# Optimization experiments

Hardware: AMD Instinct MI355X
Metric: run time of the kernel (lower is better)

## Reference

```python
import jax, jax.numpy as jnp
import numpy as np

B, N, D, R, W, H, I = 256, 2048, 128, 4, 1, 1024, 1024
CI = I + R * D                       # controller input size (1536)
IF = 2 * D * W + 2 * W + 1 + 4 * R + D * R   # interface size (787)
OPI = H + R * D                      # output_proj input (1536)


def _norm(v):
    # F.normalize(dim=-1): x / max(||x||, eps)
    return v / jnp.maximum(jnp.linalg.norm(v, axis=-1, keepdims=True), 1e-12)


def setup_inputs() -> dict:
    key = jax.random.key(0)
    ks = jax.random.split(key, 16)
    u = lambda k, shape, fan: jax.random.uniform(k, shape, jnp.float32, -1.0 / np.sqrt(fan), 1.0 / np.sqrt(fan))
    return {
        "x": jax.random.normal(ks[0], (B, I), jnp.float32),
        "memory": jax.random.normal(ks[1], (N, D), jnp.float32) * np.sqrt(2.0 / (N + D)),  # xavier-ish
        "usage": jax.random.uniform(ks[2], (N,), jnp.float32),          # usage in [0,1)
        "link": jax.random.normal(ks[3], (N, N), jnp.float32) * 0.01,   # non-trivial link state
        "W_ih": u(ks[4], (4 * H, CI), H),
        "W_hh": u(ks[5], (4 * H, H), H),
        "b_ih": u(ks[6], (4 * H,), H),
        "b_hh": u(ks[7], (4 * H,), H),
        "W_if": u(ks[8], (IF, H), H),
        "b_if": u(ks[9], (IF,), H),
        "W_out": u(ks[10], (H, OPI), OPI),
        "b_out": u(ks[11], (H,), OPI),
    }


def reference(x, memory, usage, link, W_ih, W_hh, b_ih, b_hh, W_if, b_if, W_out, b_out):
    # initial uniform read weights (prev state at first step)
    prev_rw = jnp.full((B, R, N), 1.0 / N, x.dtype)
    read_flat = (prev_rw @ memory).reshape(B, -1)                 # (B, R*D)
    cin = jnp.concatenate([x, read_flat], axis=-1)                # (B, CI)

    # single LSTM step, h0 = c0 = 0, torch gate order i,f,g,o
    g = cin @ W_ih.T + b_ih + b_hh
    gi, gf, gg, go = jnp.split(g, 4, axis=-1)
    c = jax.nn.sigmoid(gi) * jnp.tanh(gg)
    h = jax.nn.sigmoid(go) * jnp.tanh(c)                          # (B, H) controller out

    itf = h @ W_if.T + b_if                                       # (B, IF)
    o = 0
    write_vals = itf[:, o:o + D * W].reshape(B, W, D); o += D * W
    erase = jax.nn.sigmoid(itf[:, o:o + D * W]).reshape(B, W, D); o += D * W
    write_gates = jax.nn.sigmoid(itf[:, o:o + W]); o += W         # (B, W)
    alloc_gate = jax.nn.sigmoid(itf[:, o:o + 1]); o += 1          # (B, 1)
    o += W                                                        # free gates (parsed, unused)
    read_modes = jax.nn.softmax(itf[:, o:o + 3 * R].reshape(B, R, 3), -1); o += 3 * R
    read_str = jax.nn.softplus(itf[:, o:o + R]); o += R           # (B, R)
    read_keys = itf[:, o:o + D * R].reshape(B, R, D)

    # content addressing for the write (strength = 1)
    mem_n = _norm(memory)
    cw = jax.nn.softmax(_norm(write_vals.mean(1)) @ mem_n.T, -1)  # (B, N)

    # allocation weighting: sorted-usage cumprod (per source semantics)
    idx = jnp.argsort(usage)
    su = usage[idx]
    cp = jnp.cumprod(1.0 - su)
    alloc_s = jnp.concatenate([su[:1], su[1:] * cp[:-1]])
    alloc = jnp.zeros_like(usage).at[idx].set(alloc_s)[None, :] * alloc_gate  # (B, N)

    write_w = write_gates[:, :, None] * (0.5 * cw + 0.5 * alloc)[:, None, :]  # (B, W, N)

    # temporal link update: batch-mean of diag-masked outer product, decay 0.9
    lu = jnp.einsum('bwn,bwm->nm', write_w, write_w) / B
    lu = lu * (1.0 - jnp.eye(N, dtype=lu.dtype))
    link_new = link * 0.9 + lu * 0.1

    # memory write (erase then add, batch-mean)
    ev = erase * write_gates[:, :, None]
    av = write_vals * write_gates[:, :, None]
    erase_mat = jnp.einsum('bwn,bwd->nd', write_w, ev) / B
    add_mat = jnp.einsum('bwn,bwd->nd', write_w, av) / B
    mem_new = memory * (1.0 - erase_mat) + add_mat

    # read addressing on updated memory and updated link (all R heads vectorized)
    sim = jnp.einsum('brd,nd->brn', _norm(read_keys), _norm(mem_new))
    content_r = jax.nn.softmax(sim * read_str[:, :, None], -1)    # (B, R, N)
    backward_w = jnp.einsum('brn,nm->brm', prev_rw, link_new)     # mode 1: prev @ L
    forward_w = jnp.einsum('brn,mn->brm', prev_rw, link_new)      # mode 2: prev @ L^T
    new_rw = (read_modes[..., 0:1] * content_r
              + read_modes[..., 1:2] * backward_w
              + read_modes[..., 2:3] * forward_w)                 # (B, R, N)

    read_out = (new_rw @ mem_new).reshape(B, -1)                  # (B, R*D)
    out = jnp.concatenate([h, read_out], axis=-1) @ W_out.T + b_out
    return out
```

## Files before the change

### kernel.cpp

```cpp
#include <hip/hip_runtime.h>
#include <cmath>

#define DEVI __device__ __forceinline__

DEVI float sigm(float x){ return 1.f/(1.f+expf(-x)); }

typedef __attribute__((ext_vector_type(8))) _Float16 half8;
typedef __attribute__((ext_vector_type(4))) _Float16 half4;
typedef __attribute__((ext_vector_type(4))) float float4v;


__global__ void k_zero(float* __restrict__ p, int n){
  int i = blockIdx.x*256 + threadIdx.x;
  if (i < n) p[i] = 0.f;
}

__global__ __launch_bounds__(256) void k_stage1(
    const float* __restrict__ mem, float* __restrict__ cm, _Float16* __restrict__ mem_h)
{
  __shared__ float smem[4][132];
  const int blk = blockIdx.x, t = threadIdx.x;
  const int wv = t >> 6, lane = t & 63;
  int rbase = blk*16 + wv*4;
  float x0[4], x1[4], ss[4];
  #pragma unroll
  for (int u = 0; u < 4; u++){
    const float* a = mem + (size_t)(rbase+u)*128;
    x0[u] = a[lane]; x1[u] = a[lane+64];
  }
  #pragma unroll
  for (int u = 0; u < 4; u++) ss[u] = x0[u]*x0[u] + x1[u]*x1[u];
  #pragma unroll
  for (int o = 1; o < 64; o <<= 1){
    #pragma unroll
    for (int u = 0; u < 4; u++) ss[u] += __shfl_xor(ss[u], o);
  }
  float c0 = 0.f, c1 = 0.f;
  #pragma unroll
  for (int u = 0; u < 4; u++){
    float invn = 1.f / fmaxf(sqrtf(ss[u]), 1e-12f);
    mem_h[(size_t)(rbase+u)*128 + lane]      = (_Float16)(x0[u]*invn);
    mem_h[(size_t)(rbase+u)*128 + 64 + lane] = (_Float16)(x1[u]*invn);
    c0 += x0[u]; c1 += x1[u];
  }
  smem[wv][lane] = c0; smem[wv][64+lane] = c1;
  __syncthreads();
  if (t < 128) atomicAdd(&cm[t], smem[0][t]+smem[1][t]+smem[2][t]+smem[3][t]);
}

#define QA 264
#define QB 520
#define QB3 776

template<typename TB> struct BReg;
template<> struct BReg<_Float16>{
  half8 v;
  DEVI void load(const _Float16* p){ v = *(const half8*)p; }
  DEVI half8 get() const { return v; }
};
template<> struct BReg<float>{
  float4v a, b;
  DEVI void load(const float* p){ a = *(const float4v*)p; b = *(const float4v*)(p+4); }
  DEVI half8 get() const {
    half8 h;
    #pragma unroll
    for (int j = 0; j < 4; j++){ h[j] = (_Float16)a[j]; h[4+j] = (_Float16)b[j]; }
    return h;
  }
};

struct ARegX {
  float4v a, b; float sc;
  DEVI void load(const float* __restrict__ x, const float* __restrict__ cm, int row, int k){
    const float* p;
    if (k < 1024){ p = x + (size_t)row*1024 + k; sc = 1.f; }
    else         { p = cm + ((k - 1024) & 127); sc = (1.f/2048.f); }
    a = *(const float4v*)p; b = *(const float4v*)(p+4);
  }
  DEVI half8 get() const {
    half8 h;
    #pragma unroll
    for (int j = 0; j < 4; j++){ h[j] = (_Float16)(a[j]*sc); h[4+j] = (_Float16)(b[j]*sc); }
    return h;
  }
};

template<typename TB>
__global__ __launch_bounds__(256) void gemm_t(
    const _Float16* __restrict__ A, const TB* __restrict__ Bm, float* __restrict__ C,
    int M, int N, int K,
    const float* __restrict__ bias1, const float* __restrict__ bias2)
{
  __shared__ _Float16 Ah[2][8*QA];
  __shared__ _Float16 Bh[2][8*QB];
  const int tid = threadIdx.x;
  const int m0 = blockIdx.y*32, n0 = blockIdx.x*64;
  const int T = K >> 6;
  const int arow = tid >> 3, aq = tid & 7;
  const int brow = tid >> 3, bq = tid & 7;
  int nB0 = n0 + brow;      if (nB0 >= N) nB0 = N - 1;
  int nB1 = n0 + brow + 32; if (nB1 >= N) nB1 = N - 1;
  const _Float16* Aptr = A + (size_t)(m0 + arow)*K + aq*8;
  const TB* Bp0 = Bm + (size_t)nB0*K + bq*8;
  const TB* Bp1 = Bm + (size_t)nB1*K + bq*8;
  const int wA  = aq*QA + arow*8;
  const int wB0 = bq*QB + brow*8;
  const int wB1 = bq*QB + (brow+32)*8;
  const int wv_ = tid >> 6, lane = tid & 63;
  const int fq = lane >> 4, fr = lane & 15;
  const int m16 = (wv_ & 1)*16, nb = (wv_ >> 1)*32;

  half8 ra0, ra1;
  BReg<TB> rb00, rb10, rb01, rb11;
  ra0 = *(const half8*)(Aptr);
  rb00.load(Bp0); rb10.load(Bp1);
  if (T > 1){
    ra1 = *(const half8*)(Aptr + 64);
    rb01.load(Bp0 + 64); rb11.load(Bp1 + 64);
  }
  *(half8*)&Ah[0][wA]  = ra0;
  *(half8*)&Bh[0][wB0] = rb00.get();
  *(half8*)&Bh[0][wB1] = rb10.get();
  __syncthreads();

  float4v acc0 = {0.f,0.f,0.f,0.f}, acc1 = {0.f,0.f,0.f,0.f};
  for (int t = 0; t < T; t++){
    const int cur = t & 1, nxt = cur ^ 1;
    if (t+2 < T){
      if (cur == 0){
        ra0 = *(const half8*)(Aptr + (t+2)*64);
        rb00.load(Bp0 + (t+2)*64); rb10.load(Bp1 + (t+2)*64);
      } else {
        ra1 = *(const half8*)(Aptr + (t+2)*64);
        rb01.load(Bp0 + (t+2)*64); rb11.load(Bp1 + (t+2)*64);
      }
    }
    #pragma unroll
    for (int s = 0; s < 2; s++){
      int q = s*4 + fq;
      half8 a  = *(half8*)&Ah[cur][q*QA + (m16+fr)*8];
      half8 b0 = *(half8*)&Bh[cur][q*QB + (nb+fr)*8];
      half8 b1 = *(half8*)&Bh[cur][q*QB + (nb+16+fr)*8];
      acc0 = __builtin_amdgcn_mfma_f32_16x16x32_f16(a, b0, acc0, 0, 0, 0);
      acc1 = __builtin_amdgcn_mfma_f32_16x16x32_f16(a, b1, acc1, 0, 0, 0);
    }
    if (t+1 < T){
      if (nxt == 1){
        *(half8*)&Ah[1][wA]  = ra1;
        *(half8*)&Bh[1][wB0] = rb01.get();
        *(half8*)&Bh[1][wB1] = rb11.get();
      } else {
        *(half8*)&Ah[0][wA]  = ra0;
        *(half8*)&Bh[0][wB0] = rb00.get();
        *(half8*)&Bh[0][wB1] = rb10.get();
      }
    }
    __syncthreads();
  }

  const int colA = n0 + nb + fr, colB = colA + 16;
  #pragma unroll
  for (int i = 0; i < 4; i++){
    int m = m0 + m16 + fq*4 + i;
    if (colA < N){
      float v = acc0[i];
      if (bias1) v += bias1[colA];
      if (bias2) v += bias2[colA];
      C[(size_t)m*N + colA] = v;
    }
    if (colB < N){
      float v = acc1[i];
      if (bias1) v += bias1[colB];
      if (bias2) v += bias2[colB];
      C[(size_t)m*N + colB] = v;
    }
  }
}

__global__ __launch_bounds__(256) void gemm_hro(
    const _Float16* __restrict__ Ah_, const _Float16* __restrict__ Aro,
    const float* __restrict__ Bm, float* __restrict__ C,
    const float* __restrict__ bias1)
{
  __shared__ _Float16 Ah[2][8*QA];
  __shared__ _Float16 Bh[2][8*QB];
  const int tid = threadIdx.x;
  const int m0 = blockIdx.y*32, n0 = blockIdx.x*64;
  const int T = 24;
  const int arow = tid >> 3, aq = tid & 7;
  const int brow = tid >> 3, bq = tid & 7;
  const int arw = m0 + arow;
  const float* Bp0 = Bm + (size_t)(n0 + brow)*1536 + bq*8;
  const float* Bp1 = Bm + (size_t)(n0 + brow + 32)*1536 + bq*8;
  const int wA  = aq*QA + arow*8;
  const int wB0 = bq*QB + brow*8;
  const int wB1 = bq*QB + (brow+32)*8;
  const int wv_ = tid >> 6, lane = tid & 63;
  const int fq = lane >> 4, fr = lane & 15;
  const int m16 = (wv_ & 1)*16, nb = (wv_ >> 1)*32;

  auto ldA = [&](int k) -> half8 {
    const _Float16* p = (k < 1024) ? (Ah_ + (size_t)arw*1024 + k)
                                   : (Aro + (size_t)arw*512 + (k - 1024));
    return *(const half8*)p;
  };

  half8 ra0, ra1;
  BReg<float> rb00, rb10, rb01, rb11;
  ra0 = ldA(aq*8);
  rb00.load(Bp0); rb10.load(Bp1);
  ra1 = ldA(aq*8 + 64);
  rb01.load(Bp0 + 64); rb11.load(Bp1 + 64);
  *(half8*)&Ah[0][wA]  = ra0;
  *(half8*)&Bh[0][wB0] = rb00.get();
  *(half8*)&Bh[0][wB1] = rb10.get();
  __syncthreads();

  float4v acc0 = {0.f,0.f,0.f,0.f}, acc1 = {0.f,0.f,0.f,0.f};
  for (int t = 0; t < T; t++){
    const int cur = t & 1, nxt = cur ^ 1;
    if (t+2 < T){
      if (cur == 0){
        ra0 = ldA(aq*8 + (t+2)*64);
        rb00.load(Bp0 + (t+2)*64); rb10.load(Bp1 + (t+2)*64);
      } else {
        ra1 = ldA(aq*8 + (t+2)*64);
        rb01.load(Bp0 + (t+2)*64); rb11.load(Bp1 + (t+2)*64);
      }
    }
    #pragma unroll
    for (int s = 0; s < 2; s++){
      int q = s*4 + fq;
      half8 a  = *(half8*)&Ah[cur][q*QA + (m16+fr)*8];
      half8 b0 = *(half8*)&Bh[cur][q*QB + (nb+fr)*8];
      half8 b1 = *(half8*)&Bh[cur][q*QB + (nb+16+fr)*8];
      acc0 = __builtin_amdgcn_mfma_f32_16x16x32_f16(a, b0, acc0, 0, 0, 0);
      acc1 = __builtin_amdgcn_mfma_f32_16x16x32_f16(a, b1, acc1, 0, 0, 0);
    }
    if (t+1 < T){
      if (nxt == 1){
        *(half8*)&Ah[1][wA]  = ra1;
        *(half8*)&Bh[1][wB0] = rb01.get();
        *(half8*)&Bh[1][wB1] = rb11.get();
      } else {
        *(half8*)&Ah[0][wA]  = ra0;
        *(half8*)&Bh[0][wB0] = rb00.get();
        *(half8*)&Bh[0][wB1] = rb10.get();
      }
    }
    __syncthreads();
  }

  const int colA = n0 + nb + fr, colB = colA + 16;
  #pragma unroll
  for (int i = 0; i < 4; i++){
    int m = m0 + m16 + fq*4 + i;
    C[(size_t)m*1024 + colA] = acc0[i] + bias1[colA];
    C[(size_t)m*1024 + colB] = acc1[i] + bias1[colB];
  }
}

__global__ __launch_bounds__(256) void k_gemm_wwExp(
    const _Float16* __restrict__ A, const _Float16* __restrict__ Bm,
    float* __restrict__ C, float* __restrict__ rsum)
{
  __shared__ _Float16 Ah[2][8*QA];
  __shared__ _Float16 Bh[2][8*QB];
  const int tid = threadIdx.x;
  const int m0 = blockIdx.y*32, n0 = blockIdx.x*64;
  const int arow = tid >> 3, aq = tid & 7;
  const int brow = tid >> 3, bq = tid & 7;
  const _Float16* Aptr = A + (size_t)(m0 + arow)*128 + aq*8;
  const _Float16* Bp0 = Bm + (size_t)(n0 + brow)*128 + bq*8;
  const _Float16* Bp1 = Bm + (size_t)(n0 + brow + 32)*128 + bq*8;
  const int wA  = aq*QA + arow*8;
  const int wB0 = bq*QB + brow*8;
  const int wB1 = bq*QB + (brow+32)*8;
  const int wv_ = tid >> 6, lane = tid & 63;
  const int fq = lane >> 4, fr = lane & 15;
  const int m16 = (wv_ & 1)*16, nb = (wv_ >> 1)*32;

  half8 ra  = *(const half8*)(Aptr);
  half8 rb0 = *(const half8*)(Bp0);
  half8 rb1 = *(const half8*)(Bp1);
  *(half8*)&Ah[0][wA]  = ra;
  *(half8*)&Bh[0][wB0] = rb0;
  *(half8*)&Bh[0][wB1] = rb1;
  __syncthreads();

  float4v acc0 = {0.f,0.f,0.f,0.f}, acc1 = {0.f,0.f,0.f,0.f};
  for (int t = 0; t < 2; t++){
    const int cur = t & 1, nxt = cur ^ 1;
    if (t == 0){
      ra  = *(const half8*)(Aptr + 64);
      rb0 = *(const half8*)(Bp0 + 64);
      rb1 = *(const half8*)(Bp1 + 64);
    }
    #pragma unroll
    for (int s = 0; s < 2; s++){
      int q = s*4 + fq;
      half8 a  = *(half8*)&Ah[cur][q*QA + (m16+fr)*8];
      half8 b0 = *(half8*)&Bh[cur][q*QB + (nb+fr)*8];
      half8 b1 = *(half8*)&Bh[cur][q*QB + (nb+16+fr)*8];
      acc0 = __builtin_amdgcn_mfma_f32_16x16x32_f16(a, b0, acc0, 0, 0, 0);
      acc1 = __builtin_amdgcn_mfma_f32_16x16x32_f16(a, b1, acc1, 0, 0, 0);
    }
    if (t == 0){
      *(half8*)&Ah[nxt][wA]  = ra;
      *(half8*)&Bh[nxt][wB0] = rb0;
      *(half8*)&Bh[nxt][wB1] = rb1;
    }
    __syncthreads();
  }

  const int colA = n0 + nb + fr, colB = colA + 16;
  #pragma unroll
  for (int i = 0; i < 4; i++){
    int m = m0 + m16 + fq*4 + i;
    float e0 = expf(acc0[i]);
    float e1 = expf(acc1[i]);
    C[(size_t)m*2048 + colA] = e0;
    C[(size_t)m*2048 + colB] = e1;
    float rs = e0 + e1;
    #pragma unroll
    for (int o = 1; o < 16; o <<= 1) rs += __shfl_xor(rs, o);
    if (fr == 0) atomicAdd(&rsum[m], rs);
  }
}

__global__ __launch_bounds__(256) void k_big2(
    const float* __restrict__ x, const float* __restrict__ cm,
    const float* __restrict__ W,
    const float* __restrict__ b_ih, const float* __restrict__ b_hh,
    _Float16* __restrict__ h,
    const float* __restrict__ usage, float* __restrict__ alloc,
    const float* __restrict__ link, float* __restrict__ rsl, float* __restrict__ cslp)
{
  extern __shared__ char smraw[];
  const int blk = blockIdx.x, tid = threadIdx.x;
  const int wv = tid >> 6, lane = tid & 63;

  if (blk < 256){
    _Float16* AhP = (_Float16*)smraw;
    _Float16* BhP = (_Float16*)(smraw + 2*8*QA*sizeof(_Float16));
    const int SA = 8*QA, SB = 8*QB3;
    const int m0 = (blk >> 5)*32, c0 = (blk & 31)*32;
    const int T = 24;
    const int arow = tid >> 3, aq = tid & 7;
    const int brow = tid >> 3, bq = tid & 7;
    const int arw = m0 + arow;
    const float* Bpi = W + (size_t)(       c0 + brow)*1536 + bq*8;
    const float* Bpg = W + (size_t)(2048 + c0 + brow)*1536 + bq*8;
    const float* Bpo = W + (size_t)(3072 + c0 + brow)*1536 + bq*8;
    const int wA  = aq*QA + arow*8;
    const int wBi = bq*QB3 + brow*8;
    const int wBg = bq*QB3 + (32+brow)*8;
    const int wBo = bq*QB3 + (64+brow)*8;
    const int fq = lane >> 4, fr = lane & 15;
    const int m16 = (wv & 1)*16, c16 = (wv >> 1)*16;

    ARegX ax0, ax1;
    BReg<float> ri0, rg0, ro0, ri1, rg1, ro1;
    ax0.load(x, cm, arw, aq*8);
    ri0.load(Bpi); rg0.load(Bpg); ro0.load(Bpo);
    ax1.load(x, cm, arw, aq*8 + 64);
    ri1.load(Bpi + 64); rg1.load(Bpg + 64); ro1.load(Bpo + 64);
    *(half8*)&AhP[wA]  = ax0.get();
    *(half8*)&BhP[wBi] = ri0.get();
    *(half8*)&BhP[wBg] = rg0.get();
    *(half8*)&BhP[wBo] = ro0.get();
    __syncthreads();

    float4v acci = {0.f,0.f,0.f,0.f}, accg = {0.f,0.f,0.f,0.f}, acco = {0.f,0.f,0.f,0.f};
    for (int t = 0; t < T; t++){
      const int cur = t & 1, nxt = cur ^ 1;
      if (t+2 < T){
        if (cur == 0){
          ax0.load(x, cm, arw, aq*8 + (t+2)*64);
          ri0.load(Bpi + (t+2)*64); rg0.load(Bpg + (t+2)*64); ro0.load(Bpo + (t+2)*64);
        } else {
          ax1.load(x, cm, arw, aq*8 + (t+2)*64);
          ri1.load(Bpi + (t+2)*64); rg1.load(Bpg + (t+2)*64); ro1.load(Bpo + (t+2)*64);
        }
      }
      #pragma unroll
      for (int s = 0; s < 2; s++){
        int q = s*4 + fq;
        half8 a  = *(half8*)&AhP[cur*SA + q*QA + (m16+fr)*8];
        half8 bi = *(half8*)&BhP[cur*SB + q*QB3 + (c16+fr)*8];
        half8 bg = *(half8*)&BhP[cur*SB + q*QB3 + (32+c16+fr)*8];
        half8 bo = *(half8*)&BhP[cur*SB + q*QB3 + (64+c16+fr)*8];
        acci = __builtin_amdgcn_mfma_f32_16x16x32_f16(a, bi, acci, 0, 0, 0);
        accg = __builtin_amdgcn_mfma_f32_16x16x32_f16(a, bg, accg, 0, 0, 0);
        acco = __builtin_amdgcn_mfma_f32_16x16x32_f16(a, bo, acco, 0, 0, 0);
      }
      if (t+1 < T){
        if (nxt == 1){
          *(half8*)&AhP[SA + wA]  = ax1.get();
          *(half8*)&BhP[SB + wBi] = ri1.get();
          *(half8*)&BhP[SB + wBg] = rg1.get();
          *(half8*)&BhP[SB + wBo] = ro1.get();
        } else {
          *(half8*)&AhP[wA]  = ax0.get();
          *(half8*)&BhP[wBi] = ri0.get();
          *(half8*)&BhP[wBg] = rg0.get();
          *(half8*)&BhP[wBo] = ro0.get();
        }
      }
      __syncthreads();
    }

    const int col = c0 + c16 + fr;
    const float bi1 = b_ih[col]        + b_hh[col];
    const float bg1 = b_ih[2048 + col] + b_hh[2048 + col];
    const float bo1 = b_ih[3072 + col] + b_hh[3072 + col];
    #pragma unroll
    for (int i = 0; i < 4; i++){
      int m = m0 + m16 + fq*4 + i;
      float gi = acci[i] + bi1;
      float gg = accg[i] + bg1;
      float go = acco[i] + bo1;
      float c = sigm(gi) * tanhf(gg);
      h[(size_t)m*1024 + col] = (_Float16)(sigm(go) * tanhf(c));
    }
  } else if (blk < 512){
    float (*smem)[132] = (float(*)[132])smraw;
    int pb = blk - 256;
    int r0 = pb*8;
    int c0 = tid*8;
    float4v v0[8], v1[8];
    #pragma unroll
    for (int u = 0; u < 8; u++){
      const float* lp = link + (size_t)(r0+u)*2048 + c0;
      v0[u] = *(const float4v*)lp;
      v1[u] = *(const float4v*)(lp+4);
    }
    float colacc[8];
    #pragma unroll
    for (int j = 0; j < 8; j++) colacc[j] = 0.f;
    float rowpart[8];
    #pragma unroll
    for (int u = 0; u < 8; u++){
      float s = 0.f;
      #pragma unroll
      for (int j = 0; j < 4; j++){
        colacc[j]   += v0[u][j]; colacc[4+j] += v1[u][j];
        s += v0[u][j] + v1[u][j];
      }
      rowpart[u] = s;
    }
    #pragma unroll
    for (int o = 1; o < 64; o <<= 1){
      #pragma unroll
      for (int u = 0; u < 8; u++) rowpart[u] += __shfl_xor(rowpart[u], o);
    }
    if (lane == 0){
      #pragma unroll
      for (int u = 0; u < 8; u++) smem[wv][u] = rowpart[u];
    }
    __syncthreads();
    if (tid < 8) rsl[r0+tid] = smem[0][tid]+smem[1][tid]+smem[2][tid]+smem[3][tid];
    float4v w0, w1;
    #pragma unroll
    for (int j = 0; j < 4; j++){ w0[j] = colacc[j]; w1[j] = colacc[4+j]; }
    *(float4v*)&cslp[(size_t)pb*2048 + c0]     = w0;
    *(float4v*)&cslp[(size_t)pb*2048 + c0 + 4] = w1;
  } else {
    int n = (blk - 512)*4 + wv;
    float un = usage[n];
    float prod = 1.f;
    #pragma unroll
    for (int i = 0; i < 32; i++){
      int m = lane + i*64;
      float um = usage[m];
      bool before = (um < un) || (um == un && m < n);
      prod *= before ? (1.f - um) : 1.f;
    }
    #pragma unroll
    for (int o = 32; o > 0; o >>= 1) prod *= __shfl_xor(prod, o);
    if (lane == 0) alloc[n] = un * prod;
  }
}

DEVI float blockReduce128(float v, float* lds2){
  #pragma unroll
  for (int o = 32; o > 0; o >>= 1) v += __shfl_xor(v, o);
  int w = threadIdx.x >> 6;
  __syncthreads();
  if ((threadIdx.x & 63) == 0) lds2[w] = v;
  __syncthreads();
  return lds2[0] + lds2[1];
}

__global__ __launch_bounds__(128) void k_parse(const float* __restrict__ itf,
    _Float16* __restrict__ wv_h, float* __restrict__ ev, float* __restrict__ av,
    float* __restrict__ wg_, float* __restrict__ ag_,
    float* __restrict__ rm0, float* __restrict__ rm1, float* __restrict__ rm2,
    _Float16* __restrict__ rks_h)
{
  __shared__ float red[2];
  int b = blockIdx.x, t = threadIdx.x;
  const float* it = itf + (size_t)b*787;
  float wg = sigm(it[256]);
  float ag = sigm(it[257]);
  if (t == 0){ wg_[b] = wg; ag_[b] = ag; }
  float w = it[t];
  av[b*128 + t] = w * wg;
  ev[b*128 + t] = sigm(it[128 + t]) * wg;
  float ss = blockReduce128(w*w, red);
  float invwv = 1.f / fmaxf(sqrtf(ss), 1e-12f);
  wv_h[b*128 + t] = (_Float16)(w * invwv);
  if (t < 4){
    int rr = t;
    float m0v = it[259 + rr*3 + 0], m1v = it[259 + rr*3 + 1], m2v = it[259 + rr*3 + 2];
    float mx = fmaxf(m0v, fmaxf(m1v, m2v));
    float e0 = expf(m0v - mx), e1 = expf(m1v - mx), e2 = expf(m2v - mx);
    float inv = 1.f / (e0 + e1 + e2);
    rm0[b*4 + rr] = e0*inv; rm1[b*4 + rr] = e1*inv; rm2[b*4 + rr] = e2*inv;
  }
  #pragma unroll
  for (int rr = 0; rr < 4; rr++){
    float kv = it[275 + rr*128 + t];
    float ks = blockReduce128(kv*kv, red);
    float sx = it[271 + rr];
    float str = fmaxf(sx, 0.f) + log1pf(expf(-fabsf(sx)));
    float invk = 1.f / fmaxf(sqrtf(ks), 1e-12f);
    rks_h[((size_t)b*4 + rr)*128 + t] = (_Float16)(kv * invk * str);
  }
}

__global__ __launch_bounds__(256) void k_memupdate_fused(const float* __restrict__ ww,
    const float* __restrict__ ev, const float* __restrict__ av,
    const float* __restrict__ mem,
    const float* __restrict__ wg, const float* __restrict__ ag,
    const float* __restrict__ alloc, const float* __restrict__ rsum,
    const float* __restrict__ rsl, const float* __restrict__ cslp,
    _Float16* __restrict__ memn_h, _Float16* __restrict__ memnT_h,
    float* __restrict__ bwm, float* __restrict__ fwm)
{
  __shared__ float Ws[16][34];
  __shared__ float Es[16][132], Vs[16][132];
  __shared__ float lb[128], lf[128];
  __shared__ _Float16 Traw[32][132];
  __shared__ float tbs[256], c1s[256], c2s[256];
  __shared__ float allocL[32];
  __shared__ float sq[8][32], sd[8][32];
  __shared__ float cpart[8][32];
  __shared__ float bwL[32], fwL[32];
  __shared__ float sred[4];
  const int n0 = blockIdx.x*32;
  const int tid = threadIdx.x, tx = tid & 31, ty = tid >> 5;

  {
    float sa = 0.f;
    #pragma unroll
    for (int i = 0; i < 8; i++) sa += alloc[tid + i*256];
    #pragma unroll
    for (int o = 32; o > 0; o >>= 1) sa += __shfl_xor(sa, o);
    if ((tid & 63) == 0) sred[tid >> 6] = sa;
    if (tid < 128){ lb[tid] = 0.f; lf[tid] = 0.f; }
    if (tid < 32) allocL[tid] = alloc[n0 + tid];
    __syncthreads();
    sa = (sred[0]+sred[1]) + (sred[2]+sred[3]);
    float w = wg[tid], a = ag[tid];
    tbs[tid] = w*(0.5f + 0.5f*a*sa);
    c1s[tid] = 0.5f*w / rsum[tid];
    c2s[tid] = 0.5f*w*a;
  }
  {
    int col = n0 + tx;
    float s = 0.f;
    for (int p = ty*32; p < ty*32 + 32; p += 4){
      s += cslp[(size_t)(p+0)*2048 + col] + cslp[(size_t)(p+1)*2048 + col]
         + cslp[(size_t)(p+2)*2048 + col] + cslp[(size_t)(p+3)*2048 + col];
    }
    cpart[ty][tx] = s;
  }
  __syncthreads();

  const int wk = tid >> 4, wn = (tid & 15)*2;
  const int ek = tid >> 4, ec = (tid & 15)*8;
  float ae[4][4] = {}, aa[4][4] = {};
  float qp = 0.f, ddp = 0.f;
// ... 145 lines not shown
    #pragma unroll
    for (int o = 1; o < 16; o <<= 1){
      #pragma unroll
      for (int i = 0; i < 4; i++) ps[i] += __shfl_xor(ps[i], o);
    }
    #pragma unroll
    for (int i = 0; i < 4; i++) l[i] += ps[i];
    #pragma unroll
    for (int i = 0; i < 4; i++){
      Pl[wv][fq*4+i][fr]      = (_Float16)S0[i];
      Pl[wv][fq*4+i][16 + fr] = (_Float16)S1[i];
    }
    half8 pf = *(half8*)&Pl[wv][fr][fq*8];
    #pragma unroll
    for (int c = 0; c < 8; c++){
      half8 bv = *(const half8*)(Vt + (size_t)(c*16 + fr)*2048 + kb + fq*8);
      acc[c] = __builtin_amdgcn_mfma_f32_16x16x32_f16(pf, bv, acc[c], 0, 0, 0);
    }
  }
  if (fr == 0){
    #pragma unroll
    for (int i = 0; i < 4; i++){
      cmb[wv][fq*4+i]      = m[i];
      cmb[wv][16 + fq*4+i] = l[i];
    }
  }
  #pragma unroll
  for (int c = 0; c < 8; c++)
    #pragma unroll
    for (int i = 0; i < 4; i++)
      cmb[wv][32 + (fq*4+i)*128 + c*16 + fr] = acc[c][i];
  __syncthreads();
  if (tid < 16){
    float mm = fmaxf(fmaxf(cmb[0][tid], cmb[1][tid]), fmaxf(cmb[2][tid], cmb[3][tid]));
    float ll = 0.f;
    #pragma unroll
    for (int w = 0; w < 4; w++){
      float e = expf(cmb[w][tid] - mm);
      scl[w][tid] = e;
      ll += e * cmb[w][16 + tid];
    }
    pm[blockIdx.x*16 + tid] = mm;
    pl[blockIdx.x*16 + tid] = ll;
  }
  __syncthreads();
  for (int e = tid; e < 2048; e += 256){
    int q = e >> 7;
    float a = scl[0][q]*cmb[0][32+e] + scl[1][q]*cmb[1][32+e]
            + scl[2][q]*cmb[2][32+e] + scl[3][q]*cmb[3][32+e];
    pacc[(size_t)blockIdx.x*2048 + e] = a;
  }
}

__global__ void k_ro(const float* __restrict__ pacc, const float* __restrict__ pm,
                     const float* __restrict__ pl,
                     const float* __restrict__ rm0, const float* __restrict__ rm1,
                     const float* __restrict__ rm2, const float* __restrict__ bwm,
                     const float* __restrict__ fwm, _Float16* __restrict__ ro){
  int idx = blockIdx.x*256 + threadIdx.x;
  int row = idx >> 7, d = idx & 127;
  int qt = row >> 4, q = row & 15;
  float mm = -3.0e38f;
  #pragma unroll
  for (int kc = 0; kc < 8; kc++) mm = fmaxf(mm, pm[(qt*8+kc)*16 + q]);
  float num = 0.f, den = 0.f;
  #pragma unroll
  for (int kc = 0; kc < 8; kc++){
    float e = expf(pm[(qt*8+kc)*16 + q] - mm);
    den += e * pl[(qt*8+kc)*16 + q];
    num += e * pacc[(size_t)(qt*8+kc)*2048 + q*128 + d];
  }
  float pv = num / den;
  ro[idx] = (_Float16)(rm0[row]*pv + rm1[row]*bwm[d] + rm2[row]*fwm[d]);
}


extern "C" void kernel_launch(void* const* d_in, const int* in_sizes, int n_in,
                              void* d_out, int out_size, void* d_ws, size_t ws_size,
                              hipStream_t stream)
{
  const float* x     = (const float*)d_in[0];
  const float* mem   = (const float*)d_in[1];
  const float* usage = (const float*)d_in[2];
  const float* link  = (const float*)d_in[3];
  const float* W_ih  = (const float*)d_in[4];
  const float* b_ih  = (const float*)d_in[6];
  const float* b_hh  = (const float*)d_in[7];
  const float* W_if  = (const float*)d_in[8];
  const float* b_if  = (const float*)d_in[9];
  const float* W_out = (const float*)d_in[10];
  const float* b_out = (const float*)d_in[11];
  float* out = (float*)d_out;
  float* ws  = (float*)d_ws;

  float* cm     = ws + 0;
  float* bwm    = ws + 2176;
  float* fwm    = ws + 2304;
  float* rsum   = ws + 2432;
  float* wg     = ws + 6784;
  float* ag     = ws + 7040;
  float* rm0    = ws + 7296;
  float* rm1    = ws + 8320;
  float* rm2    = ws + 9344;
  float* alloc  = ws + 10368;
  float* rsl    = ws + 12416;
  float* ev     = ws + 14464;
  float* av     = ws + 47232;
  float* itf    = ws + 1128576;
  float* ww     = ws + 1330048;
  float* pacc   = ws + 1854336;
  float* pm     = ws + 2902912;
  float* pl     = ws + 2911104;
  _Float16* wv_h    = (_Float16*)(ws + 2919296);
  _Float16* mem_h   = (_Float16*)(ws + 2935680);
  _Float16* memn_h  = (_Float16*)(ws + 3066752);
  _Float16* memnT_h = (_Float16*)(ws + 3197824);
  _Float16* rks_h   = (_Float16*)(ws + 3328896);
  _Float16* ro_h    = (_Float16*)(ws + 3394432);
  _Float16* h_h     = (_Float16*)(ws + 3459968);
  float* cslp       = ws + 3591040;

  const int SH_BIG2 = (2*8*QA + 2*8*QB3) * (int)sizeof(_Float16);

  k_zero<<<11, 256, 0, stream>>>(ws, 2688);

  k_stage1<<<128, 256, 0, stream>>>(mem, cm, mem_h);

  k_big2<<<1024, 256, SH_BIG2, stream>>>(x, cm, W_ih, b_ih, b_hh, h_h,
                                         usage, alloc, link, rsl, cslp);

  gemm_t<float><<<dim3(13,8), 256, 0, stream>>>(h_h, W_if, itf, 256, 787, 1024, b_if, nullptr);
  k_parse<<<256, 128, 0, stream>>>(itf, wv_h, ev, av, wg, ag, rm0, rm1, rm2, rks_h);

  k_gemm_wwExp<<<dim3(32,8), 256, 0, stream>>>(wv_h, mem_h, ww, rsum);

  k_memupdate_fused<<<64, 256, 0, stream>>>(ww, ev, av, mem, wg, ag, alloc, rsum,
                                            rsl, cslp, memn_h, memnT_h, bwm, fwm);

  k_flash<<<512, 256, 0, stream>>>(rks_h, memn_h, memnT_h, pacc, pm, pl);

  k_ro<<<512, 256, 0, stream>>>(pacc, pm, pl, rm0, rm1, rm2, bwm, fwm, ro_h);
  gemm_hro<<<dim3(16,8), 256, 0, stream>>>(h_h, ro_h, W_out, out, b_out);

  (void)in_sizes; (void)n_in; (void)out_size; (void)ws_size;
}
```

Baseline: 230.1 us.

## Fuse stage1 into mega kernel, split LSTM read-correction, fuse readout into output GEMM

Stage1 (memory normalize and column sum) is folded into the big first kernel as extra blocks, so the LSTM GEMM no longer depends on cm and shrinks K from 1536 to 1024. The missing rank-1 read-vector contribution and the biases are applied in a new small k_lstm2 kernel that also computes the gates. The k_ro kernel is folded into gemm_hro, which computes read outputs into shared memory, dropping one launch and a global round trip. In exchange it adds a gate-preactivation buffer written and read through global memory, and each of the 16 column blocks redundantly recomputes the readout for its rows.

```diff
diff --git a/kernel.cpp b/kernel.cpp
--- a/kernel.cpp
+++ b/kernel.cpp
@@ -13,39 +13,6 @@
 __global__ void k_zero(float* __restrict__ p, int n){
   int i = blockIdx.x*256 + threadIdx.x;
   if (i < n) p[i] = 0.f;
-}
-
-__global__ __launch_bounds__(256) void k_stage1(
-    const float* __restrict__ mem, float* __restrict__ cm, _Float16* __restrict__ mem_h)
-{
-  __shared__ float smem[4][132];
-  const int blk = blockIdx.x, t = threadIdx.x;
-  const int wv = t >> 6, lane = t & 63;
-  int rbase = blk*16 + wv*4;
-  float x0[4], x1[4], ss[4];
-  #pragma unroll
-  for (int u = 0; u < 4; u++){
-    const float* a = mem + (size_t)(rbase+u)*128;
-    x0[u] = a[lane]; x1[u] = a[lane+64];
-  }
-  #pragma unroll
-  for (int u = 0; u < 4; u++) ss[u] = x0[u]*x0[u] + x1[u]*x1[u];
-  #pragma unroll
-  for (int o = 1; o < 64; o <<= 1){
-    #pragma unroll
-    for (int u = 0; u < 4; u++) ss[u] += __shfl_xor(ss[u], o);
-  }
-  float c0 = 0.f, c1 = 0.f;
-  #pragma unroll
-  for (int u = 0; u < 4; u++){
-    float invn = 1.f / fmaxf(sqrtf(ss[u]), 1e-12f);
-    mem_h[(size_t)(rbase+u)*128 + lane]      = (_Float16)(x0[u]*invn);
-    mem_h[(size_t)(rbase+u)*128 + 64 + lane] = (_Float16)(x1[u]*invn);
-    c0 += x0[u]; c1 += x1[u];
-  }
-  smem[wv][lane] = c0; smem[wv][64+lane] = c1;
-  __syncthreads();
-  if (t < 128) atomicAdd(&cm[t], smem[0][t]+smem[1][t]+smem[2][t]+smem[3][t]);
 }
 
 #define QA 264
@@ -65,22 +32,6 @@
     half8 h;
     #pragma unroll
     for (int j = 0; j < 4; j++){ h[j] = (_Float16)a[j]; h[4+j] = (_Float16)b[j]; }
-    return h;
-  }
-};
-
-struct ARegX {
-  float4v a, b; float sc;
-  DEVI void load(const float* __restrict__ x, const float* __restrict__ cm, int row, int k){
-    const float* p;
-    if (k < 1024){ p = x + (size_t)row*1024 + k; sc = 1.f; }
-    else         { p = cm + ((k - 1024) & 127); sc = (1.f/2048.f); }
-    a = *(const float4v*)p; b = *(const float4v*)(p+4);
-  }
-  DEVI half8 get() const {
-    half8 h;
-    #pragma unroll
-    for (int j = 0; j < 4; j++){ h[j] = (_Float16)(a[j]*sc); h[4+j] = (_Float16)(b[j]*sc); }
     return h;
   }
 };
@@ -177,164 +128,12 @@
   }
 }
 
-__global__ __launch_bounds__(256) void gemm_hro(
-    const _Float16* __restrict__ Ah_, const _Float16* __restrict__ Aro,
-    const float* __restrict__ Bm, float* __restrict__ C,
-    const float* __restrict__ bias1)
-{
-  __shared__ _Float16 Ah[2][8*QA];
-  __shared__ _Float16 Bh[2][8*QB];
-  const int tid = threadIdx.x;
-  const int m0 = blockIdx.y*32, n0 = blockIdx.x*64;
-  const int T = 24;
-  const int arow = tid >> 3, aq = tid & 7;
-  const int brow = tid >> 3, bq = tid & 7;
-  const int arw = m0 + arow;
-  const float* Bp0 = Bm + (size_t)(n0 + brow)*1536 + bq*8;
-  const float* Bp1 = Bm + (size_t)(n0 + brow + 32)*1536 + bq*8;
-  const int wA  = aq*QA + arow*8;
-  const int wB0 = bq*QB + brow*8;
-  const int wB1 = bq*QB + (brow+32)*8;
-  const int wv_ = tid >> 6, lane = tid & 63;
-  const int fq = lane >> 4, fr = lane & 15;
-  const int m16 = (wv_ & 1)*16, nb = (wv_ >> 1)*32;
-
-  auto ldA = [&](int k) -> half8 {
-    const _Float16* p = (k < 1024) ? (Ah_ + (size_t)arw*1024 + k)
-                                   : (Aro + (size_t)arw*512 + (k - 1024));
-    return *(const half8*)p;
-  };
-
-  half8 ra0, ra1;
-  BReg<float> rb00, rb10, rb01, rb11;
-  ra0 = ldA(aq*8);
-  rb00.load(Bp0); rb10.load(Bp1);
-  ra1 = ldA(aq*8 + 64);
-  rb01.load(Bp0 + 64); rb11.load(Bp1 + 64);
-  *(half8*)&Ah[0][wA]  = ra0;
-  *(half8*)&Bh[0][wB0] = rb00.get();
-  *(half8*)&Bh[0][wB1] = rb10.get();
-  __syncthreads();
-
-  float4v acc0 = {0.f,0.f,0.f,0.f}, acc1 = {0.f,0.f,0.f,0.f};
-  for (int t = 0; t < T; t++){
-    const int cur = t & 1, nxt = cur ^ 1;
-    if (t+2 < T){
-      if (cur == 0){
-        ra0 = ldA(aq*8 + (t+2)*64);
-        rb00.load(Bp0 + (t+2)*64); rb10.load(Bp1 + (t+2)*64);
-      } else {
-        ra1 = ldA(aq*8 + (t+2)*64);
-        rb01.load(Bp0 + (t+2)*64); rb11.load(Bp1 + (t+2)*64);
-      }
-    }
-    #pragma unroll
-    for (int s = 0; s < 2; s++){
-      int q = s*4 + fq;
-      half8 a  = *(half8*)&Ah[cur][q*QA + (m16+fr)*8];
-      half8 b0 = *(half8*)&Bh[cur][q*QB + (nb+fr)*8];
-      half8 b1 = *(half8*)&Bh[cur][q*QB + (nb+16+fr)*8];
-      acc0 = __builtin_amdgcn_mfma_f32_16x16x32_f16(a, b0, acc0, 0, 0, 0);
-      acc1 = __builtin_amdgcn_mfma_f32_16x16x32_f16(a, b1, acc1, 0, 0, 0);
-    }
-    if (t+1 < T){
-      if (nxt == 1){
-        *(half8*)&Ah[1][wA]  = ra1;
-        *(half8*)&Bh[1][wB0] = rb01.get();
-        *(half8*)&Bh[1][wB1] = rb11.get();
-      } else {
-        *(half8*)&Ah[0][wA]  = ra0;
-        *(half8*)&Bh[0][wB0] = rb00.get();
-        *(half8*)&Bh[0][wB1] = rb10.get();
-      }
-    }
-    __syncthreads();
-  }
-
-  const int colA = n0 + nb + fr, colB = colA + 16;
-  #pragma unroll
-  for (int i = 0; i < 4; i++){
-    int m = m0 + m16 + fq*4 + i;
-    C[(size_t)m*1024 + colA] = acc0[i] + bias1[colA];
-    C[(size_t)m*1024 + colB] = acc1[i] + bias1[colB];
-  }
-}
-
-__global__ __launch_bounds__(256) void k_gemm_wwExp(
-    const _Float16* __restrict__ A, const _Float16* __restrict__ Bm,
-    float* __restrict__ C, float* __restrict__ rsum)
-{
-  __shared__ _Float16 Ah[2][8*QA];
-  __shared__ _Float16 Bh[2][8*QB];
-  const int tid = threadIdx.x;
-  const int m0 = blockIdx.y*32, n0 = blockIdx.x*64;
-  const int arow = tid >> 3, aq = tid & 7;
-  const int brow = tid >> 3, bq = tid & 7;
-  const _Float16* Aptr = A + (size_t)(m0 + arow)*128 + aq*8;
-  const _Float16* Bp0 = Bm + (size_t)(n0 + brow)*128 + bq*8;
-  const _Float16* Bp1 = Bm + (size_t)(n0 + brow + 32)*128 + bq*8;
-  const int wA  = aq*QA + arow*8;
-  const int wB0 = bq*QB + brow*8;
-  const int wB1 = bq*QB + (brow+32)*8;
-  const int wv_ = tid >> 6, lane = tid & 63;
-  const int fq = lane >> 4, fr = lane & 15;
-  const int m16 = (wv_ & 1)*16, nb = (wv_ >> 1)*32;
-
-  half8 ra  = *(const half8*)(Aptr);
-  half8 rb0 = *(const half8*)(Bp0);
-  half8 rb1 = *(const half8*)(Bp1);
-  *(half8*)&Ah[0][wA]  = ra;
-  *(half8*)&Bh[0][wB0] = rb0;
-  *(half8*)&Bh[0][wB1] = rb1;
-  __syncthreads();
-
-  float4v acc0 = {0.f,0.f,0.f,0.f}, acc1 = {0.f,0.f,0.f,0.f};
-  for (int t = 0; t < 2; t++){
-    const int cur = t & 1, nxt = cur ^ 1;
-    if (t == 0){
-      ra  = *(const half8*)(Aptr + 64);
-      rb0 = *(const half8*)(Bp0 + 64);
-      rb1 = *(const half8*)(Bp1 + 64);
-    }
-    #pragma unroll
-    for (int s = 0; s < 2; s++){
-      int q = s*4 + fq;
-      half8 a  = *(half8*)&Ah[cur][q*QA + (m16+fr)*8];
-      half8 b0 = *(half8*)&Bh[cur][q*QB + (nb+fr)*8];
-      half8 b1 = *(half8*)&Bh[cur][q*QB + (nb+16+fr)*8];
-      acc0 = __builtin_amdgcn_mfma_f32_16x16x32_f16(a, b0, acc0, 0, 0, 0);
-      acc1 = __builtin_amdgcn_mfma_f32_16x16x32_f16(a, b1, acc1, 0, 0, 0);
-    }
-    if (t == 0){
-      *(half8*)&Ah[nxt][wA]  = ra;
-      *(half8*)&Bh[nxt][wB0] = rb0;
-      *(half8*)&Bh[nxt][wB1] = rb1;
-    }
-    __syncthreads();
-  }
-
-  const int colA = n0 + nb + fr, colB = colA + 16;
-  #pragma unroll
-  for (int i = 0; i < 4; i++){
-    int m = m0 + m16 + fq*4 + i;
-    float e0 = expf(acc0[i]);
-    float e1 = expf(acc1[i]);
-    C[(size_t)m*2048 + colA] = e0;
-    C[(size_t)m*2048 + colB] = e1;
-    float rs = e0 + e1;
-    #pragma unroll
-    for (int o = 1; o < 16; o <<= 1) rs += __shfl_xor(rs, o);
-    if (fr == 0) atomicAdd(&rsum[m], rs);
-  }
-}
-
-__global__ __launch_bounds__(256) void k_big2(
-    const float* __restrict__ x, const float* __restrict__ cm,
-    const float* __restrict__ W,
-    const float* __restrict__ b_ih, const float* __restrict__ b_hh,
-    _Float16* __restrict__ h,
+__global__ __launch_bounds__(256) void k_mega1(
+    const float* __restrict__ x, const float* __restrict__ W,
+    float* __restrict__ gp,
     const float* __restrict__ usage, float* __restrict__ alloc,
-    const float* __restrict__ link, float* __restrict__ rsl, float* __restrict__ cslp)
+    const float* __restrict__ link, float* __restrict__ rsl, float* __restrict__ cslp,
+    const float* __restrict__ mem, float* __restrict__ cm, _Float16* __restrict__ mem_h)
 {
   extern __shared__ char smraw[];
   const int blk = blockIdx.x, tid = threadIdx.x;
@@ -345,10 +144,10 @@
     _Float16* BhP = (_Float16*)(smraw + 2*8*QA*sizeof(_Float16));
     const int SA = 8*QA, SB = 8*QB3;
     const int m0 = (blk >> 5)*32, c0 = (blk & 31)*32;
-    const int T = 24;
+    const int T = 16;
     const int arow = tid >> 3, aq = tid & 7;
     const int brow = tid >> 3, bq = tid & 7;
-    const int arw = m0 + arow;
+    const float* Ap  = x + (size_t)(m0 + arow)*1024 + aq*8;
     const float* Bpi = W + (size_t)(       c0 + brow)*1536 + bq*8;
     const float* Bpg = W + (size_t)(2048 + c0 + brow)*1536 + bq*8;
     const float* Bpo = W + (size_t)(3072 + c0 + brow)*1536 + bq*8;
@@ -359,11 +158,10 @@
     const int fq = lane >> 4, fr = lane & 15;
     const int m16 = (wv & 1)*16, c16 = (wv >> 1)*16;
 
-    ARegX ax0, ax1;
-    BReg<float> ri0, rg0, ro0, ri1, rg1, ro1;
-    ax0.load(x, cm, arw, aq*8);
+    BReg<float> ax0, ax1, ri0, rg0, ro0, ri1, rg1, ro1;
+    ax0.load(Ap);
     ri0.load(Bpi); rg0.load(Bpg); ro0.load(Bpo);
-    ax1.load(x, cm, arw, aq*8 + 64);
+    ax1.load(Ap + 64);
     ri1.load(Bpi + 64); rg1.load(Bpg + 64); ro1.load(Bpo + 64);
     *(half8*)&AhP[wA]  = ax0.get();
     *(half8*)&BhP[wBi] = ri0.get();
@@ -376,10 +174,10 @@
       const int cur = t & 1, nxt = cur ^ 1;
       if (t+2 < T){
         if (cur == 0){
-          ax0.load(x, cm, arw, aq*8 + (t+2)*64);
+          ax0.load(Ap + (t+2)*64);
           ri0.load(Bpi + (t+2)*64); rg0.load(Bpg + (t+2)*64); ro0.load(Bpo + (t+2)*64);
         } else {
-          ax1.load(x, cm, arw, aq*8 + (t+2)*64);
+          ax1.load(Ap + (t+2)*64);
           ri1.load(Bpi + (t+2)*64); rg1.load(Bpg + (t+2)*64); ro1.load(Bpo + (t+2)*64);
         }
       }
@@ -411,17 +209,12 @@
     }
 
     const int col = c0 + c16 + fr;
-    const float bi1 = b_ih[col]        + b_hh[col];
-    const float bg1 = b_ih[2048 + col] + b_hh[2048 + col];
-    const float bo1 = b_ih[3072 + col] + b_hh[3072 + col];
     #pragma unroll
     for (int i = 0; i < 4; i++){
       int m = m0 + m16 + fq*4 + i;
-      float gi = acci[i] + bi1;
-      float gg = accg[i] + bg1;
-      float go = acco[i] + bo1;
-      float c = sigm(gi) * tanhf(gg);
-      h[(size_t)m*1024 + col] = (_Float16)(sigm(go) * tanhf(c));
+      gp[(size_t)m*1024 + col]          = acci[i];
+      gp[262144 + (size_t)m*1024 + col] = accg[i];
+      gp[524288 + (size_t)m*1024 + col] = acco[i];
     }
   } else if (blk < 512){
     float (*smem)[132] = (float(*)[132])smraw;
@@ -465,7 +258,7 @@
     for (int j = 0; j < 4; j++){ w0[j] = colacc[j]; w1[j] = colacc[4+j]; }
     *(float4v*)&cslp[(size_t)pb*2048 + c0]     = w0;
     *(float4v*)&cslp[(size_t)pb*2048 + c0 + 4] = w1;
-  } else {
+  } else if (blk < 1024){
     int n = (blk - 512)*4 + wv;
     float un = usage[n];
     float prod = 1.f;
@@ -479,6 +272,77 @@
     #pragma unroll
     for (int o = 32; o > 0; o >>= 1) prod *= __shfl_xor(prod, o);
     if (lane == 0) alloc[n] = un * prod;
+  } else {
+    float (*smem)[132] = (float(*)[132])smraw;
+    int rbase = (blk - 1024)*16 + wv*4;
+    float x0[4], x1[4], ss[4];
+    #pragma unroll
+    for (int u = 0; u < 4; u++){
+      const float* a = mem + (size_t)(rbase+u)*128;
+      x0[u] = a[lane]; x1[u] = a[lane+64];
+    }
+    #pragma unroll
+    for (int u = 0; u < 4; u++) ss[u] = x0[u]*x0[u] + x1[u]*x1[u];
+    #pragma unroll
+    for (int o = 1; o < 64; o <<= 1){
+      #pragma unroll
+      for (int u = 0; u < 4; u++) ss[u] += __shfl_xor(ss[u], o);
+    }
+    float c0s = 0.f, c1s = 0.f;
+    #pragma unroll
+    for (int u = 0; u < 4; u++){
+      float invn = 1.f / fmaxf(sqrtf(ss[u]), 1e-12f);
+      mem_h[(size_t)(rbase+u)*128 + lane]      = (_Float16)(x0[u]*invn);
+      mem_h[(size_t)(rbase+u)*128 + 64 + lane] = (_Float16)(x1[u]*invn);
+      c0s += x0[u]; c1s += x1[u];
+    }
+    smem[wv][lane] = c0s; smem[wv][64+lane] = c1s;
+    __syncthreads();
+    if (tid < 128) atomicAdd(&cm[tid], smem[0][tid]+smem[1][tid]+smem[2][tid]+smem[3][tid]);
+  }
+}
+
+__global__ __launch_bounds__(256) void k_lstm2(
+    const float* __restrict__ gp, const float* __restrict__ W,
+    const float* __restrict__ cm,
+    const float* __restrict__ b_ih, const float* __restrict__ b_hh,
+    _Float16* __restrict__ h)
+{
+  __shared__ float corrL[3][8];
+  __shared__ float cmL[128];
+  const int blk = blockIdx.x, tid = threadIdx.x;
+  const int wv = tid >> 6, lane = tid & 63;
+  const int c0 = blk*8;
+  if (tid < 128) cmL[tid] = cm[tid] * (1.f/2048.f);
+  __syncthreads();
+  for (int r = wv; r < 24; r += 4){
+    int gate = r >> 3, cc = r & 7;
+    int off = (gate == 0) ? 0 : ((gate == 1) ? 2048 : 3072);
+    int wrow = off + c0 + cc;
+    const float* wp = W + (size_t)wrow*1536 + 1024 + lane*8;
+    float4v v0 = *(const float4v*)wp;
+    float4v v1 = *(const float4v*)(wp+4);
+    float s = 0.f;
+    #pragma unroll
+    for (int j = 0; j < 4; j++){
+      s += v0[j]*cmL[(lane*8+j)   & 127];
+      s += v1[j]*cmL[(lane*8+4+j) & 127];
+    }
+    #pragma unroll
+    for (int o = 1; o < 64; o <<= 1) s += __shfl_xor(s, o);
+    if (lane == 0) corrL[gate][cc] = s + b_ih[wrow] + b_hh[wrow];
+  }
+  __syncthreads();
+  const int cc = tid & 7, br = tid >> 3;
+  const float ci = corrL[0][cc], cg = corrL[1][cc], co = corrL[2][cc];
+  for (int it = 0; it < 8; it++){
+    int b = br*8 + it;
+    size_t off = (size_t)b*1024 + c0 + cc;
+    float gi = gp[off]          + ci;
+    float gg = gp[262144 + off] + cg;
+    float go = gp[524288 + off] + co;
+    float c = sigm(gi) * tanhf(gg);
+    h[off] = (_Float16)(sigm(go) * tanhf(c));
   }
 }
 
@@ -529,6 +393,74 @@
   }
 }
 
+__global__ __launch_bounds__(256) void k_gemm_wwExp(
+    const _Float16* __restrict__ A, const _Float16* __restrict__ Bm,
+    float* __restrict__ C, float* __restrict__ rsum)
+{
+  __shared__ _Float16 Ah[2][8*QA];
+  __shared__ _Float16 Bh[2][8*QB];
+  const int tid = threadIdx.x;
+  const int m0 = blockIdx.y*32, n0 = blockIdx.x*64;
+  const int arow = tid >> 3, aq = tid & 7;
+  const int brow = tid >> 3, bq = tid & 7;
+  const _Float16* Aptr = A + (size_t)(m0 + arow)*128 + aq*8;
+  const _Float16* Bp0 = Bm + (size_t)(n0 + brow)*128 + bq*8;
+  const _Float16* Bp1 = Bm + (size_t)(n0 + brow + 32)*128 + bq*8;
+  const int wA  = aq*QA + arow*8;
+  const int wB0 = bq*QB + brow*8;
+  const int wB1 = bq*QB + (brow+32)*8;
+  const int wv_ = tid >> 6, lane = tid & 63;
+  const int fq = lane >> 4, fr = lane & 15;
+  const int m16 = (wv_ & 1)*16, nb = (wv_ >> 1)*32;
+
+  half8 ra  = *(const half8*)(Aptr);
+  half8 rb0 = *(const half8*)(Bp0);
+  half8 rb1 = *(const half8*)(Bp1);
+  *(half8*)&Ah[0][wA]  = ra;
+  *(half8*)&Bh[0][wB0] = rb0;
+  *(half8*)&Bh[0][wB1] = rb1;
+  __syncthreads();
+
+  float4v acc0 = {0.f,0.f,0.f,0.f}, acc1 = {0.f,0.f,0.f,0.f};
+  for (int t = 0; t < 2; t++){
+    const int cur = t & 1, nxt = cur ^ 1;
+    if (t == 0){
+      ra  = *(const half8*)(Aptr + 64);
+      rb0 = *(const half8*)(Bp0 + 64);
+      rb1 = *(const half8*)(Bp1 + 64);
+    }
+    #pragma unroll
+    for (int s = 0; s < 2; s++){
+      int q = s*4 + fq;
+      half8 a  = *(half8*)&Ah[cur][q*QA + (m16+fr)*8];
+      half8 b0 = *(half8*)&Bh[cur][q*QB + (nb+fr)*8];
+      half8 b1 = *(half8*)&Bh[cur][q*QB + (nb+16+fr)*8];
+      acc0 = __builtin_amdgcn_mfma_f32_16x16x32_f16(a, b0, acc0, 0, 0, 0);
+      acc1 = __builtin_amdgcn_mfma_f32_16x16x32_f16(a, b1, acc1, 0, 0, 0);
+    }
+    if (t == 0){
+      *(half8*)&Ah[nxt][wA]  = ra;
+      *(half8*)&Bh[nxt][wB0] = rb0;
+      *(half8*)&Bh[nxt][wB1] = rb1;
+    }
+    __syncthreads();
+  }
+
+  const int colA = n0 + nb + fr, colB = colA + 16;
+  #pragma unroll
+  for (int i = 0; i < 4; i++){
+    int m = m0 + m16 + fq*4 + i;
+    float e0 = expf(acc0[i]);
+    float e1 = expf(acc1[i]);
+    C[(size_t)m*2048 + colA] = e0;
+    C[(size_t)m*2048 + colB] = e1;
+    float rs = e0 + e1;
+    #pragma unroll
+    for (int o = 1; o < 16; o <<= 1) rs += __shfl_xor(rs, o);
+    if (fr == 0) atomicAdd(&rsum[m], rs);
+  }
+}
+
 __global__ __launch_bounds__(256) void k_memupdate_fused(const float* __restrict__ ww,
     const float* __restrict__ ev, const float* __restrict__ av,
     const float* __restrict__ mem,
@@ -780,26 +712,126 @@
   }
 }
 
-__global__ void k_ro(const float* __restrict__ pacc, const float* __restrict__ pm,
-                     const float* __restrict__ pl,
-                     const float* __restrict__ rm0, const float* __restrict__ rm1,
-                     const float* __restrict__ rm2, const float* __restrict__ bwm,
-                     const float* __restrict__ fwm, _Float16* __restrict__ ro){
-  int idx = blockIdx.x*256 + threadIdx.x;
-  int row = idx >> 7, d = idx & 127;
-  int qt = row >> 4, q = row & 15;
-  float mm = -3.0e38f;
+__global__ __launch_bounds__(256) void gemm_hro(
+    const _Float16* __restrict__ Ah_, const float* __restrict__ Bm, float* __restrict__ C,
+    const float* __restrict__ bias1,
+    const float* __restrict__ pacc, const float* __restrict__ pm, const float* __restrict__ pl,
+    const float* __restrict__ rm0, const float* __restrict__ rm1, const float* __restrict__ rm2,
+    const float* __restrict__ bwm, const float* __restrict__ fwm)
+{
+  __shared__ _Float16 Ah[2][8*QA];
+  __shared__ _Float16 Bh[2][8*QB];
+  __shared__ _Float16 roL[32][512];
+  const int tid = threadIdx.x;
+  const int m0 = blockIdx.y*32, n0 = blockIdx.x*64;
+  const int T = 24;
+
+  {
+    int pr = tid >> 1;
+    int r = pr >> 2, rh = pr & 3;
+    int half = tid & 1;
+    int row4 = (m0 + r)*4 + rh;
+    int qt = row4 >> 4, q = row4 & 15;
+    float mm = -3.0e38f;
+    #pragma unroll
+    for (int kc = 0; kc < 8; kc++) mm = fmaxf(mm, pm[(qt*8+kc)*16 + q]);
+    float e[8]; float den = 0.f;
+    #pragma unroll
+    for (int kc = 0; kc < 8; kc++){
+      e[kc] = expf(pm[(qt*8+kc)*16 + q] - mm);
+      den += e[kc] * pl[(qt*8+kc)*16 + q];
+    }
+    float r0v = rm0[row4], r1v = rm1[row4], r2v = rm2[row4];
+    float invden = 1.f / den;
+    int d0 = half*64;
+    for (int dd = 0; dd < 64; dd += 4){
+      int d = d0 + dd;
+      float4v num = {0.f,0.f,0.f,0.f};
+      #pragma unroll
+      for (int kc = 0; kc < 8; kc++){
+        float4v pv = *(const float4v*)(pacc + (size_t)(qt*8+kc)*2048 + q*128 + d);
+        #pragma unroll
+        for (int j = 0; j < 4; j++) num[j] += e[kc]*pv[j];
+      }
+      #pragma unroll
+      for (int j = 0; j < 4; j++){
+        float pvv = num[j]*invden;
+        roL[r][rh*128 + d + j] = (_Float16)(r0v*pvv + r1v*bwm[d+j] + r2v*fwm[d+j]);
+      }
+    }
+  }
+  __syncthreads();
+
+  const int arow = tid >> 3, aq = tid & 7;
+  const int brow = tid >> 3, bq = tid & 7;
+  const int arw = m0 + arow;
+  const float* Bp0 = Bm + (size_t)(n0 + brow)*1536 + bq*8;
+  const float* Bp1 = Bm + (size_t)(n0 + brow + 32)*1536 + bq*8;
+  const int wA  = aq*QA + arow*8;
+  const int wB0 = bq*QB + brow*8;
+  const int wB1 = bq*QB + (brow+32)*8;
+  const int wv_ = tid >> 6, lane = tid & 63;
+  const int fq = lane >> 4, fr = lane & 15;
+  const int m16 = (wv_ & 1)*16, nb = (wv_ >> 1)*32;
+
+  auto ldA = [&](int k) -> half8 {
+    if (k < 1024) return *(const half8*)(Ah_ + (size_t)arw*1024 + k);
+    return *(const half8*)&roL[arow][k - 1024];
+  };
+
+  half8 ra0, ra1;
+  BReg<float> rb00, rb10, rb01, rb11;
+  ra0 = ldA(aq*8);
+  rb00.load(Bp0); rb10.load(Bp1);
+  ra1 = ldA(aq*8 + 64);
+  rb01.load(Bp0 + 64); rb11.load(Bp1 + 64);
+  *(half8*)&Ah[0][wA]  = ra0;
+  *(half8*)&Bh[0][wB0] = rb00.get();
+  *(half8*)&Bh[0][wB1] = rb10.get();
+  __syncthreads();
+
+  float4v acc0 = {0.f,0.f,0.f,0.f}, acc1 = {0.f,0.f,0.f,0.f};
+  for (int t = 0; t < T; t++){
+    const int cur = t & 1, nxt = cur ^ 1;
+    if (t+2 < T){
+      if (cur == 0){
+        ra0 = ldA(aq*8 + (t+2)*64);
+        rb00.load(Bp0 + (t+2)*64); rb10.load(Bp1 + (t+2)*64);
+      } else {
+        ra1 = ldA(aq*8 + (t+2)*64);
+        rb01.load(Bp0 + (t+2)*64); rb11.load(Bp1 + (t+2)*64);
+      }
+    }
+    #pragma unroll
+    for (int s = 0; s < 2; s++){
+      int q = s*4 + fq;
+      half8 a  = *(half8*)&Ah[cur][q*QA + (m16+fr)*8];
+      half8 b0 = *(half8*)&Bh[cur][q*QB + (nb+fr)*8];
+      half8 b1 = *(half8*)&Bh[cur][q*QB + (nb+16+fr)*8];
+      acc0 = __builtin_amdgcn_mfma_f32_16x16x32_f16(a, b0, acc0, 0, 0, 0);
+      acc1 = __builtin_amdgcn_mfma_f32_16x16x32_f16(a, b1, acc1, 0, 0, 0);
+    }
+    if (t+1 < T){
+      if (nxt == 1){
+        *(half8*)&Ah[1][wA]  = ra1;
+        *(half8*)&Bh[1][wB0] = rb01.get();
+        *(half8*)&Bh[1][wB1] = rb11.get();
+      } else {
+        *(half8*)&Ah[0][wA]  = ra0;
+        *(half8*)&Bh[0][wB0] = rb00.get();
+        *(half8*)&Bh[0][wB1] = rb10.get();
+      }
+    }
+    __syncthreads();
+  }
+
+  const int colA = n0 + nb + fr, colB = colA + 16;
   #pragma unroll
-  for (int kc = 0; kc < 8; kc++) mm = fmaxf(mm, pm[(qt*8+kc)*16 + q]);
-  float num = 0.f, den = 0.f;
-  #pragma unroll
-  for (int kc = 0; kc < 8; kc++){
-    float e = expf(pm[(qt*8+kc)*16 + q] - mm);
-    den += e * pl[(qt*8+kc)*16 + q];
-    num += e * pacc[(size_t)(qt*8+kc)*2048 + q*128 + d];
-  }
-  float pv = num / den;
-  ro[idx] = (_Float16)(rm0[row]*pv + rm1[row]*bwm[d] + rm2[row]*fwm[d]);
+  for (int i = 0; i < 4; i++){
+    int m = m0 + m16 + fq*4 + i;
+    C[(size_t)m*1024 + colA] = acc0[i] + bias1[colA];
+    C[(size_t)m*1024 + colB] = acc1[i] + bias1[colB];
+  }
 }
 
 
@@ -844,18 +876,18 @@
   _Float16* memn_h  = (_Float16*)(ws + 3066752);
   _Float16* memnT_h = (_Float16*)(ws + 3197824);
   _Float16* rks_h   = (_Float16*)(ws + 3328896);
-  _Float16* ro_h    = (_Float16*)(ws + 3394432);
   _Float16* h_h     = (_Float16*)(ws + 3459968);
   float* cslp       = ws + 3591040;
-
-  const int SH_BIG2 = (2*8*QA + 2*8*QB3) * (int)sizeof(_Float16);
+  float* gp         = ws + 4115328;
+
+  const int SH_MEGA = (2*8*QA + 2*8*QB3) * (int)sizeof(_Float16);
 
   k_zero<<<11, 256, 0, stream>>>(ws, 2688);
 
-  k_stage1<<<128, 256, 0, stream>>>(mem, cm, mem_h);
-
-  k_big2<<<1024, 256, SH_BIG2, stream>>>(x, cm, W_ih, b_ih, b_hh, h_h,
-                                         usage, alloc, link, rsl, cslp);
+  k_mega1<<<1152, 256, SH_MEGA, stream>>>(x, W_ih, gp, usage, alloc, link, rsl, cslp,
+                                          mem, cm, mem_h);
+
+  k_lstm2<<<128, 256, 0, stream>>>(gp, W_ih, cm, b_ih, b_hh, h_h);
 
   gemm_t<float><<<dim3(13,8), 256, 0, stream>>>(h_h, W_if, itf, 256, 787, 1024, b_if, nullptr);
   k_parse<<<256, 128, 0, stream>>>(itf, wv_h, ev, av, wg, ag, rm0, rm1, rm2, rks_h);
@@ -867,8 +899,8 @@
 
   k_flash<<<512, 256, 0, stream>>>(rks_h, memn_h, memnT_h, pacc, pm, pl);
 
-  k_ro<<<512, 256, 0, stream>>>(pacc, pm, pl, rm0, rm1, rm2, bwm, fwm, ro_h);
-  gemm_hro<<<dim3(16,8), 256, 0, stream>>>(h_h, ro_h, W_out, out, b_out);
+  gemm_hro<<<dim3(16,8), 256, 0, stream>>>(h_h, W_out, out, b_out,
+                                           pacc, pm, pl, rm0, rm1, rm2, bwm, fwm);
 
   (void)in_sizes; (void)n_in; (void)out_size; (void)ws_size;
 }
```

Result: slower. 242.9 us (+5.6%).
